# Optimization experiments

Hardware: AMD Instinct MI355X
Metric: run time of the kernel (lower is better)

Reference implementation:

```python
import jax, jax.numpy as jnp
import numpy as np

DIM = 1024
NUM_HEADS = 16
HEAD_DIM = DIM // NUM_HEADS
SCALING = HEAD_DIM ** (-0.5)


def setup_inputs() -> dict:
    key = jax.random.key(0)
    ks = jax.random.split(key, 9)
    B, S = 2, 2048
    s = DIM ** -0.5  # ~ torch Linear init scale
    inp = {
        "x": jax.random.normal(ks[0], (B, S, DIM), dtype=jnp.float32),
        "wq": jax.random.uniform(ks[1], (DIM, DIM), jnp.float32, -s, s),
        "bq": jax.random.uniform(ks[2], (DIM,), jnp.float32, -s, s),
        "wk": jax.random.uniform(ks[3], (DIM, DIM), jnp.float32, -s, s),
        "bk": jax.random.uniform(ks[4], (DIM,), jnp.float32, -s, s),
        "wv": jax.random.uniform(ks[5], (DIM, DIM), jnp.float32, -s, s),
        "bv": jax.random.uniform(ks[6], (DIM,), jnp.float32, -s, s),
        "wo": jax.random.uniform(ks[7], (DIM, DIM), jnp.float32, -s, s),
        "bo": jax.random.uniform(ks[8], (DIM,), jnp.float32, -s, s),
    }
    return inp


def reference(x, wq, bq, wk, bk, wv, bv, wo, bo):
    B, S, D = x.shape
    # projections (weights stored [out,in] like torch Linear -> x @ W.T + b)
    q = (x @ wq.T + bq).reshape(B, S, NUM_HEADS, HEAD_DIM)
    k = (x @ wk.T + bk).reshape(B, S, NUM_HEADS, HEAD_DIM)
    v = (x @ wv.T + bv).reshape(B, S, NUM_HEADS, HEAD_DIM)
    # [B,H,S,S] scores, scaled
    scores = jnp.einsum("bqhd,bkhd->bhqk", q, k) * SCALING
    attn = jax.nn.softmax(scores, axis=-1)
    # dropout p=0.0 (eval): identity
    out = jnp.einsum("bhqk,bkhd->bqhd", attn, v).reshape(B, S, D)
    return out @ wo.T + bo
```

## Files before the change

### kernel.cpp

```cpp
#include <hip/hip_runtime.h>

#define DIM 1024
#define NHEADS 16
#define HDIM 64
#define BATCH 2
#define SEQ 2048
#define MTOT (BATCH*SEQ)
#define QSCALE 0.18033688011112042f
#define XN ((size_t)MTOT*DIM)
#define WN ((size_t)DIM*DIM)

typedef __attribute__((ext_vector_type(8))) short short8;
typedef __attribute__((ext_vector_type(4))) float f32x4;
typedef __attribute__((ext_vector_type(16))) float f32x16;
typedef __attribute__((ext_vector_type(2))) int int2v;

static __device__ __forceinline__ unsigned short bf16rne(float f) {
    unsigned u = __builtin_bit_cast(unsigned, f);
    return (unsigned short)((u + 0x7fffu + ((u >> 16) & 1u)) >> 16);
}

static __device__ __forceinline__ void gld16(const void* g, void* l) {
    __builtin_amdgcn_global_load_lds((const __attribute__((address_space(1))) void*)g,
                                     (__attribute__((address_space(3))) void*)l, 16, 0, 0);
}

static __device__ __forceinline__ f32x16 mfma32(short8 a, short8 b, f32x16 c) {
    return __builtin_amdgcn_mfma_f32_32x32x16_bf16(a, b, c, 0, 0, 0);
}

__global__ __launch_bounds__(256)
void prep(const float* __restrict__ x, const float* __restrict__ wq, const float* __restrict__ wk,
          const float* __restrict__ wv, const float* __restrict__ wo, unsigned short* __restrict__ dst)
{
    const size_t i = ((size_t)blockIdx.x*256 + threadIdx.x)*8;
    const float* s; size_t o;
    if (i < XN)           { s = x;  o = i; }
    else if (i < XN+WN)   { s = wq; o = i - XN; }
    else if (i < XN+2*WN) { s = wk; o = i - XN - WN; }
    else if (i < XN+3*WN) { s = wv; o = i - XN - 2*WN; }
    else                  { s = wo; o = i - XN - 3*WN; }
    float4 a = *(const float4*)(s + o);
    float4 b = *(const float4*)(s + o + 4);
    uint4 w;
    w.x = (unsigned)bf16rne(a.x) | ((unsigned)bf16rne(a.y) << 16);
    w.y = (unsigned)bf16rne(a.z) | ((unsigned)bf16rne(a.w) << 16);
    w.z = (unsigned)bf16rne(b.x) | ((unsigned)bf16rne(b.y) << 16);
    w.w = (unsigned)bf16rne(b.z) | ((unsigned)bf16rne(b.w) << 16);
    *(uint4*)&dst[i] = w;
}

__global__ __launch_bounds__(256)
void gemm_qkv(const unsigned short* __restrict__ A,
              const unsigned short* __restrict__ W0, const unsigned short* __restrict__ W1,
              const unsigned short* __restrict__ W2,
              const float* __restrict__ b0, const float* __restrict__ b1, const float* __restrict__ b2,
              unsigned short* __restrict__ o0, unsigned short* __restrict__ o1, unsigned short* __restrict__ o2)
{
    __shared__ __align__(16) unsigned short smem[24576];
    #define AS(s) (smem + (s)*4096)
    #define BS(s) (smem + 12288 + (s)*4096)
    const int t = threadIdx.x, wid = t >> 6, lane = t & 63;
    const int lr = lane & 15, lg = lane >> 4;
    const int bid = blockIdx.y * 24 + blockIdx.x;
    const int swz = (bid & 7) * 96 + (bid >> 3);
    const int sx = swz % 24, sy = swz / 24;
    const int widx = sx >> 3;
    const int n0 = (sx & 7) << 7;
    const int m0 = sy << 7;
    const unsigned short* W = widx == 0 ? W0 : (widx == 1 ? W1 : W2);
    const float* bias        = widx == 0 ? b0 : (widx == 1 ? b1 : b2);

    const int wm = wid >> 1, wn = wid & 1;
    const int f0 = 2*wid, f1 = f0 + 1;
    const unsigned short* Ag0 = A + (size_t)(m0 + f0*16 + lr)*DIM + lg*8;
    const unsigned short* Ag1 = A + (size_t)(m0 + f1*16 + lr)*DIM + lg*8;
    const unsigned short* Bg0 = W + (size_t)(n0 + f0*16 + lr)*DIM + lg*8;
    const unsigned short* Bg1 = W + (size_t)(n0 + f1*16 + lr)*DIM + lg*8;

    auto stage = [&](int tt, int slot) {
        const int ko = tt * 32;
        gld16(Ag0 + ko, AS(slot) + f0*512); gld16(Ag1 + ko, AS(slot) + f1*512);
        gld16(Bg0 + ko, BS(slot) + f0*512); gld16(Bg1 + ko, BS(slot) + f1*512);
    };

    f32x4 acc[4][4] = {};
    stage(0, 0); stage(1, 1);
    int c0 = 0, c1 = 1, c2 = 2;

    for (int it = 0; it < DIM/32; ++it) {
        if (it < DIM/32 - 2) { asm volatile("s_waitcnt vmcnt(4)" ::: "memory"); }
        else                 { asm volatile("s_waitcnt vmcnt(0)" ::: "memory"); }
        __builtin_amdgcn_s_barrier();
        short8 af[4], bf[4];
        #pragma unroll
        for (int i = 0; i < 4; ++i) af[i] = *(const short8*)(AS(c0) + (wm*4+i)*512 + lane*8);
        #pragma unroll
        for (int i = 0; i < 4; ++i) bf[i] = *(const short8*)(BS(c0) + (wn*4+i)*512 + lane*8);
        if (it + 2 < DIM/32) stage(it + 2, c2);
        __builtin_amdgcn_s_setprio(1);
        #pragma unroll
        for (int mb = 0; mb < 4; ++mb)
            #pragma unroll
            for (int nb = 0; nb < 4; ++nb)
                acc[mb][nb] = __builtin_amdgcn_mfma_f32_16x16x32_bf16(af[mb], bf[nb], acc[mb][nb], 0, 0, 0);
        __builtin_amdgcn_s_setprio(0);
        const int tmp = c0; c0 = c1; c1 = c2; c2 = tmp;
    }

    if (widx == 0) {
        #pragma unroll
        for (int nb = 0; nb < 4; ++nb) {
            const int col = n0 + wn*64 + nb*16 + lr;
            const float bv = bias[col];
            #pragma unroll
            for (int mb = 0; mb < 4; ++mb) {
                #pragma unroll
                for (int j = 0; j < 4; ++j) {
                    const int row = m0 + wm*64 + mb*16 + lg*4 + j;
                    o0[(size_t)row*DIM + col] = bf16rne((acc[mb][nb][j] + bv) * QSCALE);
                }
            }
        }
    } else {
        unsigned short* outp = (widx == 1) ? o1 : o2;
        const int isV = (widx == 2);
        __syncthreads();
        unsigned short (*tile)[136] = (unsigned short (*)[136])smem;
        #pragma unroll
        for (int nb = 0; nb < 4; ++nb) {
            const int col = wn*64 + nb*16 + lr;
            const float bv = bias[n0 + col];
            #pragma unroll
            for (int mb = 0; mb < 4; ++mb) {
                #pragma unroll
                for (int j = 0; j < 4; ++j)
                    tile[wm*64 + mb*16 + lg*4 + j][col] = bf16rne(acc[mb][nb][j] + bv);
            }
        }
        __syncthreads();
        const int bb  = m0 >> 11;
        const int kt0 = (m0 & (SEQ-1)) >> 6;
        const int hh0 = n0 >> 6;
        #pragma unroll
        for (int shot = 0; shot < 8; ++shot) {
            const int idx = t + shot*256;
            const int tid = idx >> 9;
            const int fr  = (idx >> 6) & 7;
            const int ln  = idx & 63;
            const int ktl = tid & 1, hhl = tid >> 1;
            short8 ov;
            if (isV) {
                const int r0 = ktl*64 + (fr & 3)*16 + (ln >> 5)*8;
                const int c  = hhl*64 + (fr >> 2)*32 + (ln & 31);
                #pragma unroll
                for (int e = 0; e < 8; ++e) ov[e] = (short)tile[r0 + e][c];
            } else {
                const int r  = ktl*64 + (fr >> 2)*32 + (ln & 31);
                const int cc = hhl*64 + (fr & 3)*16 + (ln >> 5)*8;
                ov = *(const short8*)&tile[r][cc];
            }
            unsigned short* dst = outp
                + ((size_t)((bb*NHEADS + hh0 + hhl)*32 + kt0 + ktl))*4096 + fr*512 + ln*8;
            *(short8*)dst = ov;
        }
    }
    #undef AS
    #undef BS
}

__global__ __launch_bounds__(256)
void gemm_o(const unsigned short* __restrict__ A, const unsigned short* __restrict__ W,
            const float* __restrict__ bias, float* __restrict__ fo)
{
    __shared__ __align__(16) unsigned short As[3][2048];
    __shared__ __align__(16) unsigned short Bs[3][4096];
    const int t = threadIdx.x, wid = t >> 6, lane = t & 63;
    const int lr = lane & 15, lg = lane >> 4;
    const int bid = blockIdx.y * 8 + blockIdx.x;
    const int swz = (bid & 7) * 64 + (bid >> 3);
    const int n0 = (swz & 7) << 7;
    const int m0 = (swz >> 3) << 6;
    const int wm = wid >> 1, wn = wid & 1;

    const int fa = wid;
    const int g0 = 2*wid, g1 = g0 + 1;
    const unsigned short* Ag  = A + (size_t)(m0 + fa*16 + lr)*DIM + lg*8;
    const unsigned short* Bg0 = W + (size_t)(n0 + g0*16 + lr)*DIM + lg*8;
    const unsigned short* Bg1 = W + (size_t)(n0 + g1*16 + lr)*DIM + lg*8;

    auto stage = [&](int tt, int slot) {
        const int ko = tt * 32;
        gld16(Ag + ko, &As[slot][fa*512]);
        gld16(Bg0 + ko, &Bs[slot][g0*512]); gld16(Bg1 + ko, &Bs[slot][g1*512]);
    };

    f32x4 acc[2][4] = {};
    stage(0, 0); stage(1, 1);
    int c0 = 0, c1 = 1, c2 = 2;

    for (int it = 0; it < DIM/32; ++it) {
        if (it < DIM/32 - 2) { asm volatile("s_waitcnt vmcnt(3)" ::: "memory"); }
        else                 { asm volatile("s_waitcnt vmcnt(0)" ::: "memory"); }
        __builtin_amdgcn_s_barrier();
        short8 af[2], bf[4];
        #pragma unroll
        for (int i = 0; i < 2; ++i) af[i] = *(const short8*)&As[c0][(wm*2+i)*512 + lane*8];
        #pragma unroll
        for (int i = 0; i < 4; ++i) bf[i] = *(const short8*)&Bs[c0][(wn*4+i)*512 + lane*8];
        if (it + 2 < DIM/32) stage(it + 2, c2);
        __builtin_amdgcn_s_setprio(1);
        #pragma unroll
        for (int mb = 0; mb < 2; ++mb)
            #pragma unroll
            for (int nb = 0; nb < 4; ++nb)
                acc[mb][nb] = __builtin_amdgcn_mfma_f32_16x16x32_bf16(af[mb], bf[nb], acc[mb][nb], 0, 0, 0);
        __builtin_amdgcn_s_setprio(0);
        const int tmp = c0; c0 = c1; c1 = c2; c2 = tmp;
    }

    #pragma unroll
    for (int nb = 0; nb < 4; ++nb) {
        const int col = n0 + wn*64 + nb*16 + lr;
        const float bv = bias[col];
        #pragma unroll
        for (int mb = 0; mb < 2; ++mb) {
            #pragma unroll
            for (int j = 0; j < 4; ++j) {
                const int row = m0 + wm*32 + mb*16 + lg*4 + j;
                fo[(size_t)row*DIM + col] = acc[mb][nb][j] + bv;
            }
        }
    }
}

struct PA { short8 p[4]; };

static __device__ __forceinline__ PA softmax_pack(const f32x16& s0, const f32x16& s1, float& lsum) {
    float rsum = 0.f;
    unsigned pw0[4][2], pw1[4][2];
    #pragma unroll
    for (int r1 = 0; r1 < 4; ++r1)
        #pragma unroll
        for (int tt = 0; tt < 2; ++tt) {
            float pa_ = __builtin_amdgcn_exp2f(s0[4*r1+2*tt]);
            float pb_ = __builtin_amdgcn_exp2f(s0[4*r1+2*tt+1]);
            float pc_ = __builtin_amdgcn_exp2f(s1[4*r1+2*tt]);
            float pd_ = __builtin_amdgcn_exp2f(s1[4*r1+2*tt+1]);
            rsum += (pa_ + pb_) + (pc_ + pd_);
            asm("v_cvt_pk_bf16_f32 %0, %1, %2" : "=v"(pw0[r1][tt]) : "v"(pa_), "v"(pb_));
            asm("v_cvt_pk_bf16_f32 %0, %1, %2" : "=v"(pw1[r1][tt]) : "v"(pc_), "v"(pd_));
        }
    rsum += __shfl_xor(rsum, 32);
    lsum += rsum;
    PA r;
    #pragma unroll
    for (int ss = 0; ss < 4; ++ss) {
        union { short8 s8; unsigned u[4]; } pu;
        #pragma unroll
        for (int tt = 0; tt < 2; ++tt) {
            const unsigned a = (ss >> 1) ? pw1[2*(ss&1)][tt]   : pw0[2*(ss&1)][tt];
            const unsigned b = (ss >> 1) ? pw1[2*(ss&1)+1][tt] : pw0[2*(ss&1)+1][tt];
            int2v sw = __builtin_amdgcn_permlane32_swap((int)a, (int)b, false, false);
            pu.u[tt]     = (unsigned)sw[0];
            pu.u[2 + tt] = (unsigned)sw[1];
        }
        r.p[ss] = pu.s8;
    }
    return r;
}

__global__ __launch_bounds__(128)
void attn_mfma2(const unsigned short* __restrict__ Q, const unsigned short* __restrict__ Kp,
                const unsigned short* __restrict__ Vp, unsigned short* __restrict__ O)
{
    __shared__ __align__(16) unsigned short Ks[4][4096];
    __shared__ __align__(16) unsigned short Vs[4][4096];
    const int t = threadIdx.x, wid = t >> 6, lane = t & 63;
    const int l31 = lane & 31, h = lane >> 5;
    const int bid = blockIdx.y * 16 + blockIdx.x;
    const int swz = (bid & 7) * 64 + (bid >> 3);
    const int qt = swz & 15, bh = swz >> 4;
    const int b = bh >> 4, hh = bh & 15;
    const size_t qkbase = (size_t)b*SEQ*DIM + (size_t)hh*HDIM;
    const unsigned short* Qb = Q + qkbase;
    unsigned short*       Ob = O + qkbase;
    const int q0 = qt*128 + wid*64;

    short8 qfA[4], qfB[4];
    #pragma unroll
    for (int ds = 0; ds < 4; ++ds) {
        qfA[ds] = *(const short8*)&Qb[(size_t)(q0 + l31)*DIM + ds*16 + h*8];
        qfB[ds] = *(const short8*)&Qb[(size_t)(q0 + 32 + l31)*DIM + ds*16 + h*8];
    }

    const unsigned short* Kg = Kp + (size_t)bh*32*4096 + 4*wid*512 + lane*8;
    const unsigned short* Vg = Vp + (size_t)bh*32*4096 + 4*wid*512 + lane*8;

    auto stage = [&](int tn) {
        const size_t ko = (size_t)tn * 4096;
        const int bb = tn & 3;
        #pragma unroll
        for (int i = 0; i < 4; ++i) {
            gld16(Kg + ko + i*512, &Ks[bb][(4*wid + i)*512]);
            gld16(Vg + ko + i*512, &Vs[bb][(4*wid + i)*512]);
        }
    };

    f32x16 ctxA0 = {}, ctxA1 = {}, ctxB0 = {}, ctxB1 = {};
    float lsumA = 0.0f, lsumB = 0.0f;

    stage(0); stage(1);

    const int NW = SEQ/128;
    for (int w = 0; w < NW; ++w) {
        const int t0 = 2*w;
        const int ba = t0 & 3, bb2 = (t0+1) & 3;
        const bool more = (w + 1 < NW);

        if (more) { asm volatile("s_waitcnt vmcnt(8)" ::: "memory"); }
        else      { asm volatile("s_waitcnt vmcnt(0)" ::: "memory"); }
        __builtin_amdgcn_s_barrier();
        if (more) stage(t0 + 2);

        f32x16 s0A = {}, s1A = {}, s0B = {}, s1B = {};
        __builtin_amdgcn_s_setprio(1);
        #pragma unroll
        for (int ds = 0; ds < 4; ++ds) {
            short8 kf0 = *(const short8*)&Ks[ba][ds*512 + lane*8];
            short8 kf1 = *(const short8*)&Ks[ba][(4+ds)*512 + lane*8];
            s0A = mfma32(kf0, qfA[ds], s0A);
            s1A = mfma32(kf1, qfA[ds], s1A);
            s0B = mfma32(kf0, qfB[ds], s0B);
            s1B = mfma32(kf1, qfB[ds], s1B);
        }
        __builtin_amdgcn_s_setprio(0);

        PA paA = softmax_pack(s0A, s1A, lsumA);
        PA paB = softmax_pack(s0B, s1B, lsumB);

        if (more) { asm volatile("s_waitcnt vmcnt(8)" ::: "memory"); }
        else      { asm volatile("s_waitcnt vmcnt(0)" ::: "memory"); }
        __builtin_amdgcn_s_barrier();
        if (more) stage(t0 + 3);

        f32x16 r0A = {}, r1A = {}, r0B = {}, r1B = {};
        __builtin_amdgcn_s_setprio(1);
        #pragma unroll
        for (int ds = 0; ds < 4; ++ds) {
            short8 kf0 = *(const short8*)&Ks[bb2][ds*512 + lane*8];
            short8 kf1 = *(const short8*)&Ks[bb2][(4+ds)*512 + lane*8];
            r0A = mfma32(kf0, qfA[ds], r0A);
            r1A = mfma32(kf1, qfA[ds], r1A);
            r0B = mfma32(kf0, qfB[ds], r0B);
            r1B = mfma32(kf1, qfB[ds], r1B);
        }
        #pragma unroll
        for (int ss = 0; ss < 4; ++ss) {
            short8 vf0 = *(const short8*)&Vs[ba][ss*512 + lane*8];
            short8 vf1 = *(const short8*)&Vs[ba][(4+ss)*512 + lane*8];
            ctxA0 = mfma32(paA.p[ss], vf0, ctxA0);
            ctxA1 = mfma32(paA.p[ss], vf1, ctxA1);
            ctxB0 = mfma32(paB.p[ss], vf0, ctxB0);
            ctxB1 = mfma32(paB.p[ss], vf1, ctxB1);
        }
        __builtin_amdgcn_s_setprio(0);

        PA pbA = softmax_pack(r0A, r1A, lsumA);
        PA pbB = softmax_pack(r0B, r1B, lsumB);

        __builtin_amdgcn_s_setprio(1);
        #pragma unroll
        for (int ss = 0; ss < 4; ++ss) {
            short8 vf0 = *(const short8*)&Vs[bb2][ss*512 + lane*8];
            short8 vf1 = *(const short8*)&Vs[bb2][(4+ss)*512 + lane*8];
            ctxA0 = mfma32(pbA.p[ss], vf0, ctxA0);
            ctxA1 = mfma32(pbA.p[ss], vf1, ctxA1);
            ctxB0 = mfma32(pbB.p[ss], vf0, ctxB0);
            ctxB1 = mfma32(pbB.p[ss], vf1, ctxB1);
        }
        __builtin_amdgcn_s_setprio(0);
    }

    const float linvA = 1.0f / lsumA;
    const float linvB = 1.0f / lsumB;
    #pragma unroll
    for (int r = 0; r < 16; ++r) {
        const int qrow = (r&3) + 8*(r>>2) + 4*h;
        const float nmA = __shfl(linvA, qrow);
        const float nmB = __shfl(linvB, qrow);
        unsigned short* pA = &Ob[(size_t)(q0 + qrow)*DIM + l31];
        unsigned short* pB = &Ob[(size_t)(q0 + 32 + qrow)*DIM + l31];
        pA[0]  = bf16rne(ctxA0[r] * nmA);
        pA[32] = bf16rne(ctxA1[r] * nmA);
        pB[0]  = bf16rne(ctxB0[r] * nmB);
        pB[32] = bf16rne(ctxB1[r] * nmB);
    }
}

extern "C" void kernel_launch(void* const* d_in, const int* in_sizes, int n_in,
                              void* d_out, int out_size, void* d_ws, size_t ws_size,
                              hipStream_t stream) {
    const float* x  = (const float*)d_in[0];
    const float* wq = (const float*)d_in[1];
    const float* bq = (const float*)d_in[2];
    const float* wk = (const float*)d_in[3];
    const float* bk = (const float*)d_in[4];
    const float* wv = (const float*)d_in[5];
    const float* bv = (const float*)d_in[6];
    const float* wo = (const float*)d_in[7];
    const float* bo = (const float*)d_in[8];
    float* out = (float*)d_out;

    unsigned short* Xb  = (unsigned short*)d_ws;
    unsigned short* Wqb = Xb  + XN;
    unsigned short* Wkb = Wqb + WN;
    unsigned short* Wvb = Wkb + WN;
    unsigned short* Wob = Wvb + WN;
    unsigned short* Qb  = Wob + WN;
    unsigned short* Kpb = Qb  + XN;
    unsigned short* Vpb = Kpb + XN;
    unsigned short* Cb  = Xb;

    prep<<<4096, 256, 0, stream>>>(x, wq, wk, wv, wo, Xb);

    gemm_qkv<<<dim3(24, 32), 256, 0, stream>>>(Xb, Wqb, Wkb, Wvb, bq, bk, bv, Qb, Kpb, Vpb);

    attn_mfma2<<<dim3(16, BATCH*NHEADS), 128, 0, stream>>>(Qb, Kpb, Vpb, Cb);

    gemm_o<<<dim3(8, 64), 256, 0, stream>>>(Cb, Wob, bo, out);
}
```

Baseline: 138.1 us.

## Split key tiles across wave pairs in attention with LDS reduction of partial contexts

The attention kernel moves to 512-thread blocks where each pair of waves shares a 64-query group and splits every 64-key tile in half, so each wave does half the QK and PV MFMAs per tile. Partial context accumulators and row sums are reduced through shared memory at the end before normalisation and the store. Each block now covers 256 queries, so fewer blocks share each K/V stage, and per-thread staging drops to one load per tensor per tile. This adds a final LDS reduction plus extra barriers, uses larger shared memory, and halves the grid, which may lower occupancy.

```diff
diff --git a/kernel.cpp b/kernel.cpp
--- a/kernel.cpp
+++ b/kernel.cpp
@@ -234,34 +234,30 @@
     }
 }
 
-struct PA { short8 p[4]; };
-
-static __device__ __forceinline__ PA softmax_pack(const f32x16& s0, const f32x16& s1, float& lsum) {
+struct PA2 { short8 p[2]; };
+
+static __device__ __forceinline__ PA2 smpack32(const f32x16& s0, float& lsum) {
     float rsum = 0.f;
-    unsigned pw0[4][2], pw1[4][2];
+    unsigned pw0[4][2];
     #pragma unroll
     for (int r1 = 0; r1 < 4; ++r1)
         #pragma unroll
         for (int tt = 0; tt < 2; ++tt) {
             float pa_ = __builtin_amdgcn_exp2f(s0[4*r1+2*tt]);
             float pb_ = __builtin_amdgcn_exp2f(s0[4*r1+2*tt+1]);
-            float pc_ = __builtin_amdgcn_exp2f(s1[4*r1+2*tt]);
-            float pd_ = __builtin_amdgcn_exp2f(s1[4*r1+2*tt+1]);
-            rsum += (pa_ + pb_) + (pc_ + pd_);
+            rsum += pa_ + pb_;
             asm("v_cvt_pk_bf16_f32 %0, %1, %2" : "=v"(pw0[r1][tt]) : "v"(pa_), "v"(pb_));
-            asm("v_cvt_pk_bf16_f32 %0, %1, %2" : "=v"(pw1[r1][tt]) : "v"(pc_), "v"(pd_));
         }
     rsum += __shfl_xor(rsum, 32);
     lsum += rsum;
-    PA r;
+    PA2 r;
     #pragma unroll
-    for (int ss = 0; ss < 4; ++ss) {
+    for (int ss = 0; ss < 2; ++ss) {
         union { short8 s8; unsigned u[4]; } pu;
         #pragma unroll
         for (int tt = 0; tt < 2; ++tt) {
-            const unsigned a = (ss >> 1) ? pw1[2*(ss&1)][tt]   : pw0[2*(ss&1)][tt];
-            const unsigned b = (ss >> 1) ? pw1[2*(ss&1)+1][tt] : pw0[2*(ss&1)+1][tt];
-            int2v sw = __builtin_amdgcn_permlane32_swap((int)a, (int)b, false, false);
+            int2v sw = __builtin_amdgcn_permlane32_swap(
+                (int)pw0[2*ss][tt], (int)pw0[2*ss+1][tt], false, false);
             pu.u[tt]     = (unsigned)sw[0];
             pu.u[2 + tt] = (unsigned)sw[1];
         }
@@ -270,22 +266,27 @@
     return r;
 }
 
-__global__ __launch_bounds__(128)
-void attn_mfma2(const unsigned short* __restrict__ Q, const unsigned short* __restrict__ Kp,
+__global__ __launch_bounds__(512)
+void attn_mfma3(const unsigned short* __restrict__ Q, const unsigned short* __restrict__ Kp,
                 const unsigned short* __restrict__ Vp, unsigned short* __restrict__ O)
 {
-    __shared__ __align__(16) unsigned short Ks[4][4096];
-    __shared__ __align__(16) unsigned short Vs[4][4096];
+    __shared__ __align__(16) unsigned char smem[67584];
+    unsigned short* KsB = (unsigned short*)smem;
+    unsigned short* VsB = (unsigned short*)(smem + 32768);
+    float* cb = (float*)smem;
+
     const int t = threadIdx.x, wid = t >> 6, lane = t & 63;
     const int l31 = lane & 31, h = lane >> 5;
-    const int bid = blockIdx.y * 16 + blockIdx.x;
-    const int swz = (bid & 7) * 64 + (bid >> 3);
-    const int qt = swz & 15, bh = swz >> 4;
+    const int g = wid >> 1;
+    const int kh = wid & 1;
+    const int bid = blockIdx.y * 8 + blockIdx.x;
+    const int swz = (bid & 7) * 32 + (bid >> 3);
+    const int qt = swz & 7, bh = swz >> 3;
     const int b = bh >> 4, hh = bh & 15;
     const size_t qkbase = (size_t)b*SEQ*DIM + (size_t)hh*HDIM;
     const unsigned short* Qb = Q + qkbase;
     unsigned short*       Ob = O + qkbase;
-    const int q0 = qt*128 + wid*64;
+    const int q0 = qt*256 + g*64;
 
     short8 qfA[4], qfB[4];
     #pragma unroll
@@ -294,17 +295,14 @@
         qfB[ds] = *(const short8*)&Qb[(size_t)(q0 + 32 + l31)*DIM + ds*16 + h*8];
     }
 
-    const unsigned short* Kg = Kp + (size_t)bh*32*4096 + 4*wid*512 + lane*8;
-    const unsigned short* Vg = Vp + (size_t)bh*32*4096 + 4*wid*512 + lane*8;
+    const unsigned short* Kg = Kp + (size_t)bh*32*4096 + wid*512 + lane*8;
+    const unsigned short* Vg = Vp + (size_t)bh*32*4096 + wid*512 + lane*8;
 
     auto stage = [&](int tn) {
         const size_t ko = (size_t)tn * 4096;
         const int bb = tn & 3;
-        #pragma unroll
-        for (int i = 0; i < 4; ++i) {
-            gld16(Kg + ko + i*512, &Ks[bb][(4*wid + i)*512]);
-            gld16(Vg + ko + i*512, &Vs[bb][(4*wid + i)*512]);
-        }
+        gld16(Kg + ko, KsB + bb*4096 + wid*512);
+        gld16(Vg + ko, VsB + bb*4096 + wid*512);
     };
 
     f32x16 ctxA0 = {}, ctxA1 = {}, ctxB0 = {}, ctxB1 = {};
@@ -318,83 +316,104 @@
         const int ba = t0 & 3, bb2 = (t0+1) & 3;
         const bool more = (w + 1 < NW);
 
-        if (more) { asm volatile("s_waitcnt vmcnt(8)" ::: "memory"); }
+        if (more) { asm volatile("s_waitcnt vmcnt(2)" ::: "memory"); }
         else      { asm volatile("s_waitcnt vmcnt(0)" ::: "memory"); }
         __builtin_amdgcn_s_barrier();
         if (more) stage(t0 + 2);
 
-        f32x16 s0A = {}, s1A = {}, s0B = {}, s1B = {};
+        f32x16 sA = {}, sB = {};
         __builtin_amdgcn_s_setprio(1);
         #pragma unroll
         for (int ds = 0; ds < 4; ++ds) {
-            short8 kf0 = *(const short8*)&Ks[ba][ds*512 + lane*8];
-            short8 kf1 = *(const short8*)&Ks[ba][(4+ds)*512 + lane*8];
-            s0A = mfma32(kf0, qfA[ds], s0A);
-            s1A = mfma32(kf1, qfA[ds], s1A);
-            s0B = mfma32(kf0, qfB[ds], s0B);
-            s1B = mfma32(kf1, qfB[ds], s1B);
+            short8 kf = *(const short8*)(KsB + ba*4096 + (4*kh + ds)*512 + lane*8);
+            sA = mfma32(kf, qfA[ds], sA);
+            sB = mfma32(kf, qfB[ds], sB);
         }
         __builtin_amdgcn_s_setprio(0);
 
-        PA paA = softmax_pack(s0A, s1A, lsumA);
-        PA paB = softmax_pack(s0B, s1B, lsumB);
-
-        if (more) { asm volatile("s_waitcnt vmcnt(8)" ::: "memory"); }
+        PA2 paA = smpack32(sA, lsumA);
+        PA2 paB = smpack32(sB, lsumB);
+
+        if (more) { asm volatile("s_waitcnt vmcnt(2)" ::: "memory"); }
         else      { asm volatile("s_waitcnt vmcnt(0)" ::: "memory"); }
         __builtin_amdgcn_s_barrier();
         if (more) stage(t0 + 3);
 
-        f32x16 r0A = {}, r1A = {}, r0B = {}, r1B = {};
+        f32x16 rA = {}, rB = {};
         __builtin_amdgcn_s_setprio(1);
         #pragma unroll
         for (int ds = 0; ds < 4; ++ds) {
-            short8 kf0 = *(const short8*)&Ks[bb2][ds*512 + lane*8];
-            short8 kf1 = *(const short8*)&Ks[bb2][(4+ds)*512 + lane*8];
-            r0A = mfma32(kf0, qfA[ds], r0A);
-            r1A = mfma32(kf1, qfA[ds], r1A);
-            r0B = mfma32(kf0, qfB[ds], r0B);
-            r1B = mfma32(kf1, qfB[ds], r1B);
-        }
-        #pragma unroll
-        for (int ss = 0; ss < 4; ++ss) {
-            short8 vf0 = *(const short8*)&Vs[ba][ss*512 + lane*8];
-            short8 vf1 = *(const short8*)&Vs[ba][(4+ss)*512 + lane*8];
-            ctxA0 = mfma32(paA.p[ss], vf0, ctxA0);
-            ctxA1 = mfma32(paA.p[ss], vf1, ctxA1);
-            ctxB0 = mfma32(paB.p[ss], vf0, ctxB0);
-            ctxB1 = mfma32(paB.p[ss], vf1, ctxB1);
+            short8 kf = *(const short8*)(KsB + bb2*4096 + (4*kh + ds)*512 + lane*8);
+            rA = mfma32(kf, qfA[ds], rA);
+            rB = mfma32(kf, qfB[ds], rB);
+        }
+        #pragma unroll
+        for (int ls = 0; ls < 2; ++ls) {
+            short8 vf0 = *(const short8*)(VsB + ba*4096 + (2*kh + ls)*512 + lane*8);
+            short8 vf1 = *(const short8*)(VsB + ba*4096 + (4 + 2*kh + ls)*512 + lane*8);
+            ctxA0 = mfma32(paA.p[ls], vf0, ctxA0);
+            ctxA1 = mfma32(paA.p[ls], vf1, ctxA1);
+            ctxB0 = mfma32(paB.p[ls], vf0, ctxB0);
+            ctxB1 = mfma32(paB.p[ls], vf1, ctxB1);
         }
         __builtin_amdgcn_s_setprio(0);
 
-        PA pbA = softmax_pack(r0A, r1A, lsumA);
-        PA pbB = softmax_pack(r0B, r1B, lsumB);
+        PA2 pbA = smpack32(rA, lsumA);
+        PA2 pbB = smpack32(rB, lsumB);
 
         __builtin_amdgcn_s_setprio(1);
         #pragma unroll
-        for (int ss = 0; ss < 4; ++ss) {
-            short8 vf0 = *(const short8*)&Vs[bb2][ss*512 + lane*8];
-            short8 vf1 = *(const short8*)&Vs[bb2][(4+ss)*512 + lane*8];
-            ctxA0 = mfma32(pbA.p[ss], vf0, ctxA0);
-            ctxA1 = mfma32(pbA.p[ss], vf1, ctxA1);
-            ctxB0 = mfma32(pbB.p[ss], vf0, ctxB0);
-            ctxB1 = mfma32(pbB.p[ss], vf1, ctxB1);
+        for (int ls = 0; ls < 2; ++ls) {
+            short8 vf0 = *(const short8*)(VsB + bb2*4096 + (2*kh + ls)*512 + lane*8);
+            short8 vf1 = *(const short8*)(VsB + bb2*4096 + (4 + 2*kh + ls)*512 + lane*8);
+            ctxA0 = mfma32(pbA.p[ls], vf0, ctxA0);
+            ctxA1 = mfma32(pbA.p[ls], vf1, ctxA1);
+            ctxB0 = mfma32(pbB.p[ls], vf0, ctxB0);
+            ctxB1 = mfma32(pbB.p[ls], vf1, ctxB1);
         }
         __builtin_amdgcn_s_setprio(0);
     }
 
-    const float linvA = 1.0f / lsumA;
-    const float linvB = 1.0f / lsumB;
-    #pragma unroll
-    for (int r = 0; r < 16; ++r) {
-        const int qrow = (r&3) + 8*(r>>2) + 4*h;
-        const float nmA = __shfl(linvA, qrow);
-        const float nmB = __shfl(linvB, qrow);
-        unsigned short* pA = &Ob[(size_t)(q0 + qrow)*DIM + l31];
-        unsigned short* pB = &Ob[(size_t)(q0 + 32 + qrow)*DIM + l31];
-        pA[0]  = bf16rne(ctxA0[r] * nmA);
-        pA[32] = bf16rne(ctxA1[r] * nmA);
-        pB[0]  = bf16rne(ctxB0[r] * nmB);
-        pB[32] = bf16rne(ctxB1[r] * nmB);
+    __syncthreads();
+    if (kh == 1) {
+        float* dst = cb + ((size_t)g*64 + lane)*66;
+        #pragma unroll
+        for (int r = 0; r < 16; ++r) {
+            dst[r]      = ctxA0[r];
+            dst[16 + r] = ctxA1[r];
+            dst[32 + r] = ctxB0[r];
+            dst[48 + r] = ctxB1[r];
+        }
+        dst[64] = lsumA;
+        dst[65] = lsumB;
+    }
+    __syncthreads();
+    if (kh == 0) {
+        const float* src = cb + ((size_t)g*64 + lane)*66;
+        #pragma unroll
+        for (int r = 0; r < 16; ++r) {
+            ctxA0[r] += src[r];
+            ctxA1[r] += src[16 + r];
+            ctxB0[r] += src[32 + r];
+            ctxB1[r] += src[48 + r];
+        }
+        lsumA += src[64];
+        lsumB += src[65];
+
+        const float linvA = 1.0f / lsumA;
+        const float linvB = 1.0f / lsumB;
+        #pragma unroll
+        for (int r = 0; r < 16; ++r) {
+            const int qrow = (r&3) + 8*(r>>2) + 4*h;
+            const float nmA = __shfl(linvA, qrow);
+            const float nmB = __shfl(linvB, qrow);
+            unsigned short* pA = &Ob[(size_t)(q0 + qrow)*DIM + l31];
+            unsigned short* pB = &Ob[(size_t)(q0 + 32 + qrow)*DIM + l31];
+            pA[0]  = bf16rne(ctxA0[r] * nmA);
+            pA[32] = bf16rne(ctxA1[r] * nmA);
+            pB[0]  = bf16rne(ctxB0[r] * nmB);
+            pB[32] = bf16rne(ctxB1[r] * nmB);
+        }
     }
 }
 
@@ -426,7 +445,7 @@
 
     gemm_qkv<<<dim3(24, 32), 256, 0, stream>>>(Xb, Wqb, Wkb, Wvb, bq, bk, bv, Qb, Kpb, Vpb);
 
-    attn_mfma2<<<dim3(16, BATCH*NHEADS), 128, 0, stream>>>(Qb, Kpb, Vpb, Cb);
+    attn_mfma3<<<dim3(8, BATCH*NHEADS), 512, 0, stream>>>(Qb, Kpb, Vpb, Cb);
 
     gemm_o<<<dim3(8, 64), 256, 0, stream>>>(Cb, Wob, bo, out);
 }
```

Result: faster. 127.5 us (-7.6%).
